# Kernel tuning notes

Measured on AMD Instinct MI355X. Metric: run time of the kernel, lower is better.

## Reference

```python
import jax, jax.numpy as jnp
import numpy as np

B, DIM, H, W = 64, 640, 10, 10
EPS = 1e-05


def setup_inputs() -> dict:
    key = jax.random.key(0)
    k1, _ = jax.random.split(key)
    x = jax.random.normal(k1, (B, DIM, H, W), dtype=jnp.float32)
    init_temp = 1.0 / (2 * H * W)
    temperature = jnp.log(init_temp * jnp.ones((1, 1), dtype=jnp.float32))
    return {"x": x, "temperature": temperature}


def reference(x, temperature):
    b, d, h, w = x.shape
    xf = x.reshape(b, d, h * w)                       # [B, d, n]
    gram = jnp.einsum('bdn,ben->bde', xf, xf)         # [B, d, d]
    diag = jnp.diagonal(gram, axis1=1, axis2=2)       # [B, d]
    # ones @ (gram*eye) == diag[None,:]; (gram*eye) @ ones == diag[:,None]
    dcov = diag[:, :, None] + diag[:, None, :] - 2.0 * gram
    dcov = jnp.sqrt(jnp.exp(temperature[0, 0]) * jnp.clip(dcov, 0.0) + EPS)
    # double-centering: ones-matmuls are row/col/total means scaled by d
    row = jnp.mean(dcov, axis=2, keepdims=True)       # dcov @ ones / d
    col = jnp.mean(dcov, axis=1, keepdims=True)       # ones @ dcov / d
    tot = jnp.mean(dcov, axis=(1, 2), keepdims=True)  # ones @ dcov @ ones / d^2
    centered = dcov - row - col + tot                 # [B, d, d]
    iu = jnp.triu_indices(d)
    return centered[:, iu[0], iu[1]]                  # [B, d*(d+1)/2]
```

## Files before the change

kernel.cpp:

```cpp
#include <hip/hip_runtime.h>
#include <hip/hip_bf16.h>

#define B_    64
#define DIM   640
#define TS    64
#define NT    10
#define TRI   205120
#define EPS   1e-5f
#define SQEPS 3.1622776601683794e-3f
#define KCH   16
#define TILE_U4 1024
#define TILE_B  16384

typedef __attribute__((ext_vector_type(8)))  short bf16x8;
typedef __attribute__((ext_vector_type(16))) float f32x16;

__device__ inline unsigned pk_bf16(float a, float b) {
    __hip_bfloat162 h = __float22bfloat162_rn(float2{a, b});
    return *reinterpret_cast<unsigned*>(&h);
}
__device__ inline float bfr(float x) {
    return __bfloat162float(__float2bfloat16(x));
}
__device__ inline float fsq(float x) { return __builtin_amdgcn_sqrtf(x); }

__device__ inline void gload_lds16(const void* g, void* l) {
    __builtin_amdgcn_global_load_lds(
        (const __attribute__((address_space(1))) unsigned*)g,
        (__attribute__((address_space(3))) unsigned*)l, 16, 0, 0);
}
__device__ inline void stage_tile16(const char* __restrict__ gt, char* lt,
                                    int wv, int lane) {
    #pragma unroll
    for (int it = 0; it < 4; ++it) {
        const int seg = (wv * 4 + it) * 1024;
        gload_lds16(gt + seg + lane * 16, lt + seg);
    }
}

__global__ __launch_bounds__(256) void prep_kernel(
    const float* __restrict__ x, uint4* __restrict__ img,
    float* __restrict__ dsq)
{
    const int blk = blockIdx.x;
    const int b = blk / NT, s = blk % NT;
    const int t = threadIdx.x;
    const float4* src = (const float4*)x + (size_t)(b * DIM + s * TS) * 25;
    uint4* dst = img + (size_t)blk * TILE_U4;

    #pragma unroll
    for (int ff = 0; ff < 4; ++ff) {
        const int f = t + ff * 256;
        const int r = f >> 4, c = f & 15;
        uint4 p = {0u, 0u, 0u, 0u};
        if (c <= 12) {
            float4 lo = src[(size_t)r * 25 + 2 * c];
            float4 hi = make_float4(0.f, 0.f, 0.f, 0.f);
            if (c < 12) hi = src[(size_t)r * 25 + 2 * c + 1];
            p.x = pk_bf16(lo.x, lo.y);
            p.y = pk_bf16(lo.z, lo.w);
            p.z = pk_bf16(hi.x, hi.y);
            p.w = pk_bf16(hi.z, hi.w);
        }
        dst[r * KCH + (c ^ (r & 15))] = p;
    }

    const int r = t >> 2, q = t & 3;
    float sq = 0.f;
    for (int j = q; j < 25; j += 4) {
        float4 v = src[(size_t)r * 25 + j];
        float a0 = bfr(v.x), a1 = bfr(v.y), a2 = bfr(v.z), a3 = bfr(v.w);
        sq += a0 * a0 + a1 * a1 + a2 * a2 + a3 * a3;
    }
    sq += __shfl_xor(sq, 1);
    sq += __shfl_xor(sq, 2);
    if (q == 0) dsq[b * DIM + s * TS + r] = sq;
}

__global__ __launch_bounds__(256, 4) void strip_kernel(
    const uint4* __restrict__ img, const float* __restrict__ dsq,
    const float* __restrict__ temp, float* __restrict__ rowsum_part)
{
    __shared__ uint4 xj[2][TILE_U4];
    __shared__ float dAll[DIM];
    __shared__ float rpartw[2][TS];

    const int raw = blockIdx.x;
    const int bid = (raw & 7) * 160 + (raw >> 3);
    const int b = bid / 20, rem = bid % 20;
    const int s = rem >> 1, h = rem & 1;
    const int t = threadIdx.x, wv = t >> 6, lane = t & 63;
    const int l31 = lane & 31, khalf = lane >> 5;
    const int iq = wv & 1, jq = wv >> 1;
    const float tts = expf(temp[0]);
    const char* base = (const char*)(img + (size_t)b * NT * TILE_U4);

    stage_tile16(base + (size_t)h * TILE_B, (char*)xj[0], wv, lane);
    for (int k = t; k < DIM; k += 256) dAll[k] = dsq[b * DIM + k];

    const int irow = iq * 32 + l31;
    const uint4* own = img + (size_t)(b * NT + s) * TILE_U4;
    bf16x8 ifr[7];
    #pragma unroll
    for (int kk = 0; kk < 7; ++kk) {
        const int c = kk * 2 + khalf;
        ifr[kk] = *(const bf16x8*)&own[irow * KCH + (c ^ (irow & 15))];
    }
    const float dic = dsq[b * DIM + s * TS + irow];
    const int jr = jq * 32 + l31;
    __syncthreads();

    float rsum = 0.f;
    #pragma unroll
    for (int jj = 0; jj < 5; ++jj) {
        const int jt = h + 2 * jj;
        if (jj < 4)
            stage_tile16(base + (size_t)(jt + 2) * TILE_B,
                         (char*)xj[(jj + 1) & 1], wv, lane);
        const uint4* buf = xj[jj & 1];
        bf16x8 jfr[7];
        #pragma unroll
        for (int kk = 0; kk < 7; ++kk) {
            const int c = kk * 2 + khalf;
            jfr[kk] = *(const bf16x8*)&buf[jr * KCH + (c ^ (jr & 15))];
        }
        f32x16 acc = {};
        #pragma unroll
        for (int kk = 0; kk < 7; ++kk)
            acc = __builtin_amdgcn_mfma_f32_32x32x16_bf16(jfr[kk], ifr[kk],
                                                          acc, 0, 0, 0);
        const bool dg = (jt == s);
        #pragma unroll
        for (int r = 0; r < 16; ++r) {
            const int rf = (r & 3) + 8 * (r >> 2) + 4 * khalf;
            const int jrow = jq * 32 + rf;
            const float dj = dAll[jt * TS + jrow];
            float u = dj + dic - 2.f * acc[r];
            rsum += (dg && jrow == irow)
                  ? SQEPS : fsq(tts * fmaxf(u, 0.f) + EPS);
        }
        __syncthreads();
    }

    rsum += __shfl_xor(rsum, 32);
    if (lane < 32) rpartw[jq][iq * 32 + lane] = rsum;
    __syncthreads();
    if (t < TS)
        rowsum_part[h * (B_ * DIM) + b * DIM + s * TS + t]
            = rpartw[0][t] + rpartw[1][t];
}

__global__ __launch_bounds__(256, 4) void write_kernel(
    const uint4* __restrict__ img, const float* __restrict__ dsq,
    const float* __restrict__ temp, const float* __restrict__ rowsum_part,
    float* __restrict__ out)
{
    __shared__ uint4 xjb[2][TILE_U4];
    __shared__ float e[DIM];
    __shared__ float dAll[DIM];
    __shared__ float red4[4];

    const int raw = blockIdx.x;
    const int bid = (raw & 7) * 80 + (raw >> 3);
    const int b = bid / 10, rem = bid % 10;
    const int p = rem >> 1, h = rem & 1;
    const int t = threadIdx.x, wv = t >> 6, lane = t & 63;
    const int l31 = lane & 31, khalf = lane >> 5;
    const int wm = wv >> 1, wn = wv & 1;
    const float tts = expf(temp[0]);
    const char* base = (const char*)(img + (size_t)b * NT * TILE_U4);
    const float* r0 = rowsum_part + b * DIM;
    const float* r1 = rowsum_part + (B_ * DIM) + b * DIM;

    const int jf0 = p + ((p ^ h) & 1);
    stage_tile16(base + (size_t)jf0 * TILE_B, (char*)xjb[0], wv, lane);

    float ps = 0.f;
    for (int k = t; k < DIM; k += 256) {
        float rs = r0[k] + r1[k];
        e[k] = rs;
        dAll[k] = dsq[b * DIM + k];
        ps += rs;
    }
    ps += __shfl_xor(ps, 1);  ps += __shfl_xor(ps, 2);
    ps += __shfl_xor(ps, 4);  ps += __shfl_xor(ps, 8);
    ps += __shfl_xor(ps, 16); ps += __shfl_xor(ps, 32);
    if (lane == 0) red4[wv] = ps;
    __syncthreads();
    const float tm = (red4[0] + red4[1] + red4[2] + red4[3])
                   * (1.0f / ((float)DIM * (float)DIM));
    const float invD = 1.0f / (float)DIM;
    for (int k = t; k < DIM; k += 256)
        e[k] = 0.5f * tm - e[k] * invD;
    __syncthreads();

    const int arow = wm * 32 + l31;
    const int brow = wn * 32 + l31;

    #pragma unroll
    for (int si = 0; si < 2; ++si) {
        const int s = si ? (9 - p) : p;
        const int jf = s + ((s ^ h) & 1);
        if (jf >= NT) continue;
        if (si == 1) {
            stage_tile16(base + (size_t)jf * TILE_B, (char*)xjb[0], wv, lane);
            __syncthreads();
        }
        const int i0 = s * TS;
        const uint4* ownt = img + (size_t)(b * NT + s) * TILE_U4;
        bf16x8 afr[7];
        #pragma unroll
        for (int kk = 0; kk < 7; ++kk) {
            const int c = kk * 2 + khalf;
            afr[kk] = *(const bf16x8*)&ownt[arow * KCH + (c ^ (arow & 15))];
        }

        for (int j = jf, idx = 0; j < NT; j += 2, ++idx) {
            if (j + 2 < NT)
                stage_tile16(base + (size_t)(j + 2) * TILE_B,
                             (char*)xjb[(idx + 1) & 1], wv, lane);
            const uint4* buf = xjb[idx & 1];
            bf16x8 bfr7[7];
            #pragma unroll
            for (int kk = 0; kk < 7; ++kk) {
                const int c = kk * 2 + khalf;
                bfr7[kk] = *(const bf16x8*)&buf[brow * KCH + (c ^ (brow & 15))];
            }
            f32x16 acc = {};
            #pragma unroll
            for (int kk = 0; kk < 7; ++kk)
                acc = __builtin_amdgcn_mfma_f32_32x32x16_bf16(afr[kk], bfr7[kk],
                                                              acc, 0, 0, 0);
            const int j0 = j * TS;
            const int gj = j0 + brow;
            const float djc = dAll[gj], ejc = e[gj];
            #pragma unroll
            for (int g = 0; g < 4; ++g) {
                const int rbase = wm * 32 + 8 * g + 4 * khalf;
                const float4 e4 = *(const float4*)&e[i0 + rbase];
                const float4 d4 = *(const float4*)&dAll[i0 + rbase];
                #pragma unroll
                for (int q = 0; q < 4; ++q) {
                    const int r  = 4 * g + q;
                    const int gi = i0 + rbase + q;
                    float u = ((const float*)&d4)[q] + djc - 2.f * acc[r];
                    float v = (gi == gj) ? SQEPS
                                         : fsq(tts * fmaxf(u, 0.f) + EPS);
                    float cv = v + ((const float*)&e4)[q] + ejc;
                    const unsigned lo = (unsigned)min(gi, gj);
                    const unsigned hi2 = (unsigned)max(gi, gj);
                    unsigned idx32 = (unsigned)b * TRI + lo * DIM
                                   - ((lo * (lo - 1)) >> 1) - lo + hi2;
                    out[idx32] = cv;
                }
            }
            __syncthreads();
        }
    }
}

extern "C" void kernel_launch(void* const* d_in, const int* in_sizes, int n_in,
                              void* d_out, int out_size, void* d_ws, size_t ws_size,
                              hipStream_t stream)
{
    const float* x    = (const float*)d_in[0];
    const float* temp = (const float*)d_in[1];
    float* out         = (float*)d_out;

    float* rowsum_part = (float*)d_ws;
    float* dsq         = rowsum_part + 2 * B_ * DIM;
    uint4* img         = (uint4*)(dsq + B_ * DIM);

    prep_kernel <<<B_ * NT,     256, 0, stream>>>(x, img, dsq);
    strip_kernel<<<2 * B_ * NT, 256, 0, stream>>>(img, dsq, temp, rowsum_part);
    write_kernel<<<B_ * NT,     256, 0, stream>>>(img, dsq, temp, rowsum_part, out);
}
```

Baseline: 47.69 us.

## Fuse prep, strip and write kernels into one persistent kernel with per-batch barriers

Merges the three launches into a single 640-block kernel. Blocks of the same batch synchronise through global atomic counters that are reset by a memset. Each block now computes a full row strip (10 tiles) instead of a half strip, which removes the two-part rowsum buffer. The squared-norm computation now reuses the packed bf16 values, so the input is not reloaded. The goal is to remove launch gaps and redundant loads. The risk is deadlock if not all 640 blocks are co-resident, and the per-batch spin waits are serialised.

```diff
diff --git a/kernel.cpp b/kernel.cpp
--- a/kernel.cpp
+++ b/kernel.cpp
@@ -19,8 +19,11 @@
     __hip_bfloat162 h = __float22bfloat162_rn(float2{a, b});
     return *reinterpret_cast<unsigned*>(&h);
 }
-__device__ inline float bfr(float x) {
-    return __bfloat162float(__float2bfloat16(x));
+__device__ inline float bsq(unsigned pk) {
+    union { unsigned u; float f; } a, c;
+    a.u = pk << 16;
+    c.u = pk & 0xffff0000u;
+    return a.f * a.f + c.f * c.f;
 }
 __device__ inline float fsq(float x) { return __builtin_amdgcn_sqrtf(x); }
 
@@ -38,223 +41,218 @@
     }
 }
 
-__global__ __launch_bounds__(256) void prep_kernel(
-    const float* __restrict__ x, uint4* __restrict__ img,
-    float* __restrict__ dsq)
-{
-    const int blk = blockIdx.x;
-    const int b = blk / NT, s = blk % NT;
-    const int t = threadIdx.x;
-    const float4* src = (const float4*)x + (size_t)(b * DIM + s * TS) * 25;
-    uint4* dst = img + (size_t)blk * TILE_U4;
-
-    #pragma unroll
-    for (int ff = 0; ff < 4; ++ff) {
-        const int f = t + ff * 256;
-        const int r = f >> 4, c = f & 15;
-        uint4 p = {0u, 0u, 0u, 0u};
-        if (c <= 12) {
-            float4 lo = src[(size_t)r * 25 + 2 * c];
-            float4 hi = make_float4(0.f, 0.f, 0.f, 0.f);
-            if (c < 12) hi = src[(size_t)r * 25 + 2 * c + 1];
-            p.x = pk_bf16(lo.x, lo.y);
-            p.y = pk_bf16(lo.z, lo.w);
-            p.z = pk_bf16(hi.x, hi.y);
-            p.w = pk_bf16(hi.z, hi.w);
-        }
-        dst[r * KCH + (c ^ (r & 15))] = p;
-    }
-
-    const int r = t >> 2, q = t & 3;
-    float sq = 0.f;
-    for (int j = q; j < 25; j += 4) {
-        float4 v = src[(size_t)r * 25 + j];
-        float a0 = bfr(v.x), a1 = bfr(v.y), a2 = bfr(v.z), a3 = bfr(v.w);
-        sq += a0 * a0 + a1 * a1 + a2 * a2 + a3 * a3;
-    }
-    sq += __shfl_xor(sq, 1);
-    sq += __shfl_xor(sq, 2);
-    if (q == 0) dsq[b * DIM + s * TS + r] = sq;
-}
-
-__global__ __launch_bounds__(256, 4) void strip_kernel(
-    const uint4* __restrict__ img, const float* __restrict__ dsq,
-    const float* __restrict__ temp, float* __restrict__ rowsum_part)
+__global__ __launch_bounds__(256, 4) void mega_kernel(
+    const float* __restrict__ x, const float* __restrict__ temp,
+    uint4* __restrict__ img, float* __restrict__ dsq,
+    float* __restrict__ rowsum, unsigned* __restrict__ ctrA,
+    unsigned* __restrict__ ctrB, float* __restrict__ out)
 {
     __shared__ uint4 xj[2][TILE_U4];
     __shared__ float dAll[DIM];
+    __shared__ float e[DIM];
     __shared__ float rpartw[2][TS];
+    __shared__ float red4[4];
 
     const int raw = blockIdx.x;
-    const int bid = (raw & 7) * 160 + (raw >> 3);
-    const int b = bid / 20, rem = bid % 20;
-    const int s = rem >> 1, h = rem & 1;
+    const int bid = (raw & 7) * 80 + (raw >> 3);
+    const int b = bid / NT, u = bid % NT;
     const int t = threadIdx.x, wv = t >> 6, lane = t & 63;
     const int l31 = lane & 31, khalf = lane >> 5;
-    const int iq = wv & 1, jq = wv >> 1;
     const float tts = expf(temp[0]);
+
+    {
+        const float4* src = (const float4*)x + (size_t)(b * DIM + u * TS) * 25;
+        uint4* dst = img + (size_t)(b * NT + u) * TILE_U4;
+        #pragma unroll
+        for (int ff = 0; ff < 4; ++ff) {
+            const int f = t + ff * 256;
+            const int r = f >> 4, c = f & 15;
+            uint4 p = {0u, 0u, 0u, 0u};
+            float sq = 0.f;
+            if (c <= 12) {
+                float4 lo = src[(size_t)r * 25 + 2 * c];
+                float4 hi = make_float4(0.f, 0.f, 0.f, 0.f);
+                if (c < 12) hi = src[(size_t)r * 25 + 2 * c + 1];
+                p.x = pk_bf16(lo.x, lo.y);
+                p.y = pk_bf16(lo.z, lo.w);
+                p.z = pk_bf16(hi.x, hi.y);
+                p.w = pk_bf16(hi.z, hi.w);
+                sq = bsq(p.x) + bsq(p.y) + bsq(p.z) + bsq(p.w);
+            }
+            dst[r * KCH + (c ^ (r & 15))] = p;
+            sq += __shfl_xor(sq, 1);
+            sq += __shfl_xor(sq, 2);
+            sq += __shfl_xor(sq, 4);
+            sq += __shfl_xor(sq, 8);
+            if (c == 0) dsq[b * DIM + u * TS + r] = sq;
+        }
+    }
+    __syncthreads();
+    if (t == 0)
+        __hip_atomic_fetch_add(&ctrA[b], 1u, __ATOMIC_RELEASE,
+                               __HIP_MEMORY_SCOPE_AGENT);
+
+    if (t == 0) {
+        while (__hip_atomic_load(&ctrA[b], __ATOMIC_ACQUIRE,
+                                 __HIP_MEMORY_SCOPE_AGENT) < 10u)
+            __builtin_amdgcn_s_sleep(2);
+    }
+    __syncthreads();
+
     const char* base = (const char*)(img + (size_t)b * NT * TILE_U4);
-
-    stage_tile16(base + (size_t)h * TILE_B, (char*)xj[0], wv, lane);
-    for (int k = t; k < DIM; k += 256) dAll[k] = dsq[b * DIM + k];
-
-    const int irow = iq * 32 + l31;
-    const uint4* own = img + (size_t)(b * NT + s) * TILE_U4;
-    bf16x8 ifr[7];
-    #pragma unroll
-    for (int kk = 0; kk < 7; ++kk) {
-        const int c = kk * 2 + khalf;
-        ifr[kk] = *(const bf16x8*)&own[irow * KCH + (c ^ (irow & 15))];
-    }
-    const float dic = dsq[b * DIM + s * TS + irow];
-    const int jr = jq * 32 + l31;
-    __syncthreads();
-
-    float rsum = 0.f;
-    #pragma unroll
-    for (int jj = 0; jj < 5; ++jj) {
-        const int jt = h + 2 * jj;
-        if (jj < 4)
-            stage_tile16(base + (size_t)(jt + 2) * TILE_B,
-                         (char*)xj[(jj + 1) & 1], wv, lane);
-        const uint4* buf = xj[jj & 1];
-        bf16x8 jfr[7];
+    {
+        stage_tile16(base, (char*)xj[0], wv, lane);
+        for (int k = t; k < DIM; k += 256) dAll[k] = dsq[b * DIM + k];
+
+        const int iq = wv & 1, jq = wv >> 1;
+        const int irow = iq * 32 + l31;
+        const uint4* own = img + (size_t)(b * NT + u) * TILE_U4;
+        bf16x8 ifr[7];
         #pragma unroll
         for (int kk = 0; kk < 7; ++kk) {
             const int c = kk * 2 + khalf;
-            jfr[kk] = *(const bf16x8*)&buf[jr * KCH + (c ^ (jr & 15))];
-        }
-        f32x16 acc = {};
-        #pragma unroll
-        for (int kk = 0; kk < 7; ++kk)
-            acc = __builtin_amdgcn_mfma_f32_32x32x16_bf16(jfr[kk], ifr[kk],
-                                                          acc, 0, 0, 0);
-        const bool dg = (jt == s);
-        #pragma unroll
-        for (int r = 0; r < 16; ++r) {
-            const int rf = (r & 3) + 8 * (r >> 2) + 4 * khalf;
-            const int jrow = jq * 32 + rf;
-            const float dj = dAll[jt * TS + jrow];
-            float u = dj + dic - 2.f * acc[r];
-            rsum += (dg && jrow == irow)
-                  ? SQEPS : fsq(tts * fmaxf(u, 0.f) + EPS);
-        }
-        __syncthreads();
-    }
-
-    rsum += __shfl_xor(rsum, 32);
-    if (lane < 32) rpartw[jq][iq * 32 + lane] = rsum;
-    __syncthreads();
-    if (t < TS)
-        rowsum_part[h * (B_ * DIM) + b * DIM + s * TS + t]
-            = rpartw[0][t] + rpartw[1][t];
-}
-
-__global__ __launch_bounds__(256, 4) void write_kernel(
-    const uint4* __restrict__ img, const float* __restrict__ dsq,
-    const float* __restrict__ temp, const float* __restrict__ rowsum_part,
-    float* __restrict__ out)
-{
-    __shared__ uint4 xjb[2][TILE_U4];
-    __shared__ float e[DIM];
-    __shared__ float dAll[DIM];
-    __shared__ float red4[4];
-
-    const int raw = blockIdx.x;
-    const int bid = (raw & 7) * 80 + (raw >> 3);
-    const int b = bid / 10, rem = bid % 10;
-    const int p = rem >> 1, h = rem & 1;
-    const int t = threadIdx.x, wv = t >> 6, lane = t & 63;
-    const int l31 = lane & 31, khalf = lane >> 5;
-    const int wm = wv >> 1, wn = wv & 1;
-    const float tts = expf(temp[0]);
-    const char* base = (const char*)(img + (size_t)b * NT * TILE_U4);
-    const float* r0 = rowsum_part + b * DIM;
-    const float* r1 = rowsum_part + (B_ * DIM) + b * DIM;
-
-    const int jf0 = p + ((p ^ h) & 1);
-    stage_tile16(base + (size_t)jf0 * TILE_B, (char*)xjb[0], wv, lane);
-
-    float ps = 0.f;
-    for (int k = t; k < DIM; k += 256) {
-        float rs = r0[k] + r1[k];
-        e[k] = rs;
-        dAll[k] = dsq[b * DIM + k];
-        ps += rs;
-    }
-    ps += __shfl_xor(ps, 1);  ps += __shfl_xor(ps, 2);
-    ps += __shfl_xor(ps, 4);  ps += __shfl_xor(ps, 8);
-    ps += __shfl_xor(ps, 16); ps += __shfl_xor(ps, 32);
-    if (lane == 0) red4[wv] = ps;
-    __syncthreads();
-    const float tm = (red4[0] + red4[1] + red4[2] + red4[3])
-                   * (1.0f / ((float)DIM * (float)DIM));
-    const float invD = 1.0f / (float)DIM;
-    for (int k = t; k < DIM; k += 256)
-        e[k] = 0.5f * tm - e[k] * invD;
-    __syncthreads();
-
-    const int arow = wm * 32 + l31;
-    const int brow = wn * 32 + l31;
-
-    #pragma unroll
-    for (int si = 0; si < 2; ++si) {
-        const int s = si ? (9 - p) : p;
-        const int jf = s + ((s ^ h) & 1);
-        if (jf >= NT) continue;
-        if (si == 1) {
-            stage_tile16(base + (size_t)jf * TILE_B, (char*)xjb[0], wv, lane);
-            __syncthreads();
-        }
-        const int i0 = s * TS;
-        const uint4* ownt = img + (size_t)(b * NT + s) * TILE_U4;
-        bf16x8 afr[7];
-        #pragma unroll
-        for (int kk = 0; kk < 7; ++kk) {
-            const int c = kk * 2 + khalf;
-            afr[kk] = *(const bf16x8*)&ownt[arow * KCH + (c ^ (arow & 15))];
-        }
-
-        for (int j = jf, idx = 0; j < NT; j += 2, ++idx) {
-            if (j + 2 < NT)
-                stage_tile16(base + (size_t)(j + 2) * TILE_B,
-                             (char*)xjb[(idx + 1) & 1], wv, lane);
-            const uint4* buf = xjb[idx & 1];
-            bf16x8 bfr7[7];
+            ifr[kk] = *(const bf16x8*)&own[irow * KCH + (c ^ (irow & 15))];
+        }
+        const float dic = dsq[b * DIM + u * TS + irow];
+        const int jr = jq * 32 + l31;
+        __syncthreads();
+
+        float rsum = 0.f;
+        for (int jt = 0; jt < NT; ++jt) {
+            if (jt + 1 < NT)
+                stage_tile16(base + (size_t)(jt + 1) * TILE_B,
+                             (char*)xj[(jt + 1) & 1], wv, lane);
+            const uint4* buf = xj[jt & 1];
+            bf16x8 jfr[7];
             #pragma unroll
             for (int kk = 0; kk < 7; ++kk) {
                 const int c = kk * 2 + khalf;
-                bfr7[kk] = *(const bf16x8*)&buf[brow * KCH + (c ^ (brow & 15))];
+                jfr[kk] = *(const bf16x8*)&buf[jr * KCH + (c ^ (jr & 15))];
             }
             f32x16 acc = {};
             #pragma unroll
             for (int kk = 0; kk < 7; ++kk)
-                acc = __builtin_amdgcn_mfma_f32_32x32x16_bf16(afr[kk], bfr7[kk],
+                acc = __builtin_amdgcn_mfma_f32_32x32x16_bf16(jfr[kk], ifr[kk],
                                                               acc, 0, 0, 0);
-            const int j0 = j * TS;
-            const int gj = j0 + brow;
-            const float djc = dAll[gj], ejc = e[gj];
-            #pragma unroll
-            for (int g = 0; g < 4; ++g) {
-                const int rbase = wm * 32 + 8 * g + 4 * khalf;
-                const float4 e4 = *(const float4*)&e[i0 + rbase];
-                const float4 d4 = *(const float4*)&dAll[i0 + rbase];
+            const bool dg = (jt == u);
+            #pragma unroll
+            for (int r = 0; r < 16; ++r) {
+                const int rf = (r & 3) + 8 * (r >> 2) + 4 * khalf;
+                const int jrow = jq * 32 + rf;
+                const float dj = dAll[jt * TS + jrow];
+                float uu = dj + dic - 2.f * acc[r];
+                rsum += (dg && jrow == irow)
+                      ? SQEPS : fsq(tts * fmaxf(uu, 0.f) + EPS);
+            }
+            __syncthreads();
+        }
+
+        rsum += __shfl_xor(rsum, 32);
+        if (lane < 32) rpartw[jq][iq * 32 + lane] = rsum;
+        __syncthreads();
+        if (t < TS)
+            rowsum[b * DIM + u * TS + t] = rpartw[0][t] + rpartw[1][t];
+    }
+    __syncthreads();
+    if (t == 0)
+        __hip_atomic_fetch_add(&ctrB[b], 1u, __ATOMIC_RELEASE,
+                               __HIP_MEMORY_SCOPE_AGENT);
+
+    if (t == 0) {
+        while (__hip_atomic_load(&ctrB[b], __ATOMIC_ACQUIRE,
+                                 __HIP_MEMORY_SCOPE_AGENT) < 10u)
+            __builtin_amdgcn_s_sleep(2);
+    }
+    __syncthreads();
+
+    {
+        const int p = u >> 1, h = u & 1;
+        const int wm = wv >> 1, wn = wv & 1;
+
+        const int jf0 = p + ((p ^ h) & 1);
+        stage_tile16(base + (size_t)jf0 * TILE_B, (char*)xj[0], wv, lane);
+
+        float ps = 0.f;
+        for (int k = t; k < DIM; k += 256) {
+            float rs = rowsum[b * DIM + k];
+            e[k] = rs;
+            ps += rs;
+        }
+        ps += __shfl_xor(ps, 1);  ps += __shfl_xor(ps, 2);
+        ps += __shfl_xor(ps, 4);  ps += __shfl_xor(ps, 8);
+        ps += __shfl_xor(ps, 16); ps += __shfl_xor(ps, 32);
+        if (lane == 0) red4[wv] = ps;
+        __syncthreads();
+        const float tm = (red4[0] + red4[1] + red4[2] + red4[3])
+                       * (1.0f / ((float)DIM * (float)DIM));
+        const float invD = 1.0f / (float)DIM;
+        for (int k = t; k < DIM; k += 256)
+            e[k] = 0.5f * tm - e[k] * invD;
+        __syncthreads();
+
+        const int arow = wm * 32 + l31;
+        const int brow = wn * 32 + l31;
+
+        #pragma unroll
+        for (int si = 0; si < 2; ++si) {
+            const int s = si ? (9 - p) : p;
+            const int jf = s + ((s ^ h) & 1);
+            if (jf >= NT) continue;
+            if (si == 1) {
+                stage_tile16(base + (size_t)jf * TILE_B, (char*)xj[0],
+                             wv, lane);
+                __syncthreads();
+            }
+            const int i0 = s * TS;
+            const uint4* ownt = img + (size_t)(b * NT + s) * TILE_U4;
+            bf16x8 afr[7];
+            #pragma unroll
+            for (int kk = 0; kk < 7; ++kk) {
+                const int c = kk * 2 + khalf;
+                afr[kk] = *(const bf16x8*)&ownt[arow * KCH + (c ^ (arow & 15))];
+            }
+
+            for (int j = jf, idx = 0; j < NT; j += 2, ++idx) {
+                if (j + 2 < NT)
+                    stage_tile16(base + (size_t)(j + 2) * TILE_B,
+                                 (char*)xj[(idx + 1) & 1], wv, lane);
+                const uint4* buf = xj[idx & 1];
+                bf16x8 bfr7[7];
                 #pragma unroll
-                for (int q = 0; q < 4; ++q) {
-                    const int r  = 4 * g + q;
-                    const int gi = i0 + rbase + q;
-                    float u = ((const float*)&d4)[q] + djc - 2.f * acc[r];
-                    float v = (gi == gj) ? SQEPS
-                                         : fsq(tts * fmaxf(u, 0.f) + EPS);
-                    float cv = v + ((const float*)&e4)[q] + ejc;
-                    const unsigned lo = (unsigned)min(gi, gj);
-                    const unsigned hi2 = (unsigned)max(gi, gj);
-                    unsigned idx32 = (unsigned)b * TRI + lo * DIM
-                                   - ((lo * (lo - 1)) >> 1) - lo + hi2;
-                    out[idx32] = cv;
+                for (int kk = 0; kk < 7; ++kk) {
+                    const int c = kk * 2 + khalf;
+                    bfr7[kk] = *(const bf16x8*)&buf[brow * KCH + (c ^ (brow & 15))];
                 }
-            }
-            __syncthreads();
+                f32x16 acc = {};
+                #pragma unroll
+                for (int kk = 0; kk < 7; ++kk)
+                    acc = __builtin_amdgcn_mfma_f32_32x32x16_bf16(afr[kk], bfr7[kk],
+                                                                  acc, 0, 0, 0);
+                const int j0 = j * TS;
+                const int gj = j0 + brow;
+                const float djc = dAll[gj], ejc = e[gj];
+                #pragma unroll
+                for (int g = 0; g < 4; ++g) {
+                    const int rbase = wm * 32 + 8 * g + 4 * khalf;
+                    const float4 e4 = *(const float4*)&e[i0 + rbase];
+                    const float4 d4 = *(const float4*)&dAll[i0 + rbase];
+                    #pragma unroll
+                    for (int q = 0; q < 4; ++q) {
+                        const int r  = 4 * g + q;
+                        const int gi = i0 + rbase + q;
+                        float uu = ((const float*)&d4)[q] + djc - 2.f * acc[r];
+                        float v = (gi == gj) ? SQEPS
+                                             : fsq(tts * fmaxf(uu, 0.f) + EPS);
+                        float cv = v + ((const float*)&e4)[q] + ejc;
+                        const unsigned lo = (unsigned)min(gi, gj);
+                        const unsigned hi2 = (unsigned)max(gi, gj);
+                        unsigned idx32 = (unsigned)b * TRI + lo * DIM
+                                       - ((lo * (lo - 1)) >> 1) - lo + hi2;
+                        out[idx32] = cv;
+                    }
+                }
+                __syncthreads();
+            }
         }
     }
 }
@@ -265,13 +263,15 @@
 {
     const float* x    = (const float*)d_in[0];
     const float* temp = (const float*)d_in[1];
-    float* out         = (float*)d_out;
-
-    float* rowsum_part = (float*)d_ws;
-    float* dsq         = rowsum_part + 2 * B_ * DIM;
-    uint4* img         = (uint4*)(dsq + B_ * DIM);
-
-    prep_kernel <<<B_ * NT,     256, 0, stream>>>(x, img, dsq);
-    strip_kernel<<<2 * B_ * NT, 256, 0, stream>>>(img, dsq, temp, rowsum_part);
-    write_kernel<<<B_ * NT,     256, 0, stream>>>(img, dsq, temp, rowsum_part, out);
-}
+    float* out = (float*)d_out;
+
+    unsigned* ctrA  = (unsigned*)d_ws;
+    unsigned* ctrB  = ctrA + 64;
+    float* rowsum   = (float*)(ctrB + 64);
+    float* dsq      = rowsum + B_ * DIM;
+    uint4* img      = (uint4*)(dsq + B_ * DIM);
+
+    hipMemsetAsync(ctrA, 0, 128 * sizeof(unsigned), stream);
+    mega_kernel<<<B_ * NT, 256, 0, stream>>>(x, temp, img, dsq, rowsum,
+                                             ctrA, ctrB, out);
+}
```

Result: slower. 117.4 us (+146.3%).
